# Kernel optimization log

Measured on AMD Instinct MI355X. Metric: run time of the kernel, lower is better.

## Reference

```python
import jax, jax.numpy as jnp
import numpy as np

N_HEADS = 16
HIDDEN = 1024
HEAD_SIZE = HIDDEN // N_HEADS  # 64
BATCH = 2
SEQ_LEN = 2048


def setup_inputs() -> dict:
    key = jax.random.key(0)
    k1, k2, k3 = jax.random.split(key, 3)
    x = jax.random.normal(k1, (BATCH, SEQ_LEN, HIDDEN), dtype=jnp.float32)
    # nn.Linear(hidden, 3*hidden): store weight as [in, out] for x @ W
    W_qkv = jax.random.normal(k2, (HIDDEN, 3 * HIDDEN), dtype=jnp.float32) * (HIDDEN ** -0.5)
    b_qkv = jax.random.normal(k3, (3 * HIDDEN,), dtype=jnp.float32) * 0.02
    return {"x": x, "W_qkv": W_qkv, "b_qkv": b_qkv}


def reference(x, W_qkv, b_qkv):
    B, T, D = x.shape
    nh, hs = N_HEADS, HEAD_SIZE
    scale = hs ** -0.5

    # qkv projection, then the module's exact (unusual) reshape:
    # [B,T,3D] viewed as [3,B,T,hs,nh], permuted to [3,B,nh,T,hs]
    y = x @ W_qkv + b_qkv                      # [B, T, 3D]
    qkv = y.reshape(3, B, T, hs, nh).transpose(0, 1, 4, 2, 3)  # [3,B,nh,T,hs]
    q, k, v = qkv[0], qkv[1], qkv[2]

    # KV-cache scatter with arange index over the full seq is an identity write;
    # cache.transpose(1,2) returns k, v unchanged.

    scores = jnp.einsum('bhtd,bhsd->bhts', q, k) * scale       # [B,nh,T,T]
    causal = jnp.tril(jnp.ones((T, T), dtype=bool))
    scores = jnp.where(causal[None, None], scores, -jnp.inf)
    attn = jax.nn.softmax(scores, axis=-1)
    ctx = jnp.einsum('bhts,bhsd->bhtd', attn, v)               # [B,nh,T,hs]
    # rearrange 'b h t d -> b t (h d)'; note self.o is NOT applied in forward
    return ctx.transpose(0, 2, 1, 3).reshape(B, T, nh * hs)
```

## Files before the change

### kernel.cpp

```cpp
#include <hip/hip_runtime.h>
#include <hip/hip_bf16.h>

typedef __attribute__((ext_vector_type(8))) short s8v;
typedef __attribute__((ext_vector_type(4))) short s4v;
typedef __attribute__((ext_vector_type(4))) float f4v;

__device__ __forceinline__ void g2lds16(const void* g, void* l) {
  __builtin_amdgcn_global_load_lds(
      (__attribute__((address_space(1))) void*)(g),
      (__attribute__((address_space(3))) void*)(l), 16, 0, 0);
}

__device__ __forceinline__ short f2bf(float f) {
  __hip_bfloat16 h = __float2bfloat16(f);
  return *reinterpret_cast<short*>(&h);
}

__global__ void k_prep(const float* __restrict__ x, const float* __restrict__ W,
                       __hip_bfloat16* __restrict__ xb, __hip_bfloat16* __restrict__ Wt) {
  int bx = blockIdx.x;
  if (bx < 4096) {
    int i = (bx * 256 + threadIdx.x) * 4;
    float4 v = *(const float4*)(x + i);
    __hip_bfloat16 o[4] = {__float2bfloat16(v.x), __float2bfloat16(v.y),
                           __float2bfloat16(v.z), __float2bfloat16(v.w)};
    *(uint2*)(xb + i) = *(const uint2*)(o);
  } else {
    __shared__ float tile[32][33];
    int r = bx - 4096;
    int rt = r / 96;
    int ct = r - rt * 96;
    int c0 = ct * 32, r0 = rt * 32;
    int tr = threadIdx.x >> 5, tc = threadIdx.x & 31;
#pragma unroll
    for (int i = 0; i < 32; i += 8)
      tile[tr + i][tc] = W[(size_t)(r0 + tr + i) * 3072 + c0 + tc];
    __syncthreads();
#pragma unroll
    for (int i = 0; i < 32; i += 8)
      Wt[(size_t)(c0 + tr + i) * 1024 + r0 + tc] = __float2bfloat16(tile[tc][tr + i]);
  }
}

__global__ __launch_bounds__(256) void k_gemm(const __hip_bfloat16* __restrict__ A,
                                              const __hip_bfloat16* __restrict__ Bt,
                                              const float* __restrict__ bias,
                                              __hip_bfloat16* __restrict__ Q,
                                              __hip_bfloat16* __restrict__ K,
                                              __hip_bfloat16* __restrict__ Vt) {
  __shared__ __align__(16) __hip_bfloat16 As[2][128 * 32];
  __shared__ __align__(16) __hip_bfloat16 Bs[2][128 * 32];
  const int tid = threadIdx.x;
  const int lane = tid & 63, wave = tid >> 6;
  const int m0 = blockIdx.y * 128, n0 = blockIdx.x * 128;
  const int wm = (wave & 1) * 64, wn = (wave >> 1) * 64;
  const int lrow = lane & 15;
  const int quad = lane >> 4;

  f4v acc[4][4] = {};

  auto stage = [&](int k0, int kb) {
#pragma unroll
    for (int c = 0; c < 2; ++c) {
      int e = c * 2048 + tid * 8;
      int row = e >> 5;
      int slot = (e & 31) >> 3;
      int src = k0 + ((slot ^ ((row >> 1) & 3)) << 3);
      g2lds16(A + (size_t)(m0 + row) * 1024 + src, &As[kb][e]);
      g2lds16(Bt + (size_t)(n0 + row) * 1024 + src, &Bs[kb][e]);
    }
  };

  const int swz = (quad ^ ((lrow >> 1) & 3)) * 8;

  stage(0, 0);
  for (int it = 0; it < 32; ++it) {
    __syncthreads();
    if (it < 31) stage((it + 1) * 32, (it + 1) & 1);
    const __hip_bfloat16* Ab = As[it & 1];
    const __hip_bfloat16* Bb = Bs[it & 1];
    s8v af[4], bfr[4];
#pragma unroll
    for (int mi = 0; mi < 4; ++mi) af[mi] = *(const s8v*)(Ab + (wm + mi * 16 + lrow) * 32 + swz);
#pragma unroll
    for (int ni = 0; ni < 4; ++ni) bfr[ni] = *(const s8v*)(Bb + (wn + ni * 16 + lrow) * 32 + swz);
#pragma unroll
    for (int mi = 0; mi < 4; ++mi)
#pragma unroll
      for (int ni = 0; ni < 4; ++ni)
        acc[mi][ni] = __builtin_amdgcn_mfma_f32_16x16x32_bf16(af[mi], bfr[ni], acc[mi][ni], 0, 0, 0);
  }

  const int cw = n0 + wn;
  const int c10 = cw >> 10;
  const int d0 = (cw & 1023) >> 4;
  const int h = lrow;
  float bv[4];
#pragma unroll
  for (int ni = 0; ni < 4; ++ni) bv[ni] = bias[cw + ni * 16 + lrow];

#pragma unroll
  for (int mi = 0; mi < 4; ++mi) {
    int rbase = m0 + wm + mi * 16 + quad * 4;
#pragma unroll
    for (int reg = 0; reg < 4; ++reg) {
      int rr = rbase + reg;
      int u = 3 * rr + c10;
      int s = u >> 12;
      int b = (u >> 11) & 1;
      int t = u & 2047;
      if (s < 2) {
        __hip_bfloat16* dst = (s == 0) ? Q : K;
        s4v pk;
#pragma unroll
        for (int ni = 0; ni < 4; ++ni) pk[ni] = f2bf(acc[mi][ni][reg] + bv[ni]);
        *(s4v*)(dst + ((size_t)(b * 16 + h) * 2048 + t) * 64 + d0) = pk;
      } else {
#pragma unroll
        for (int ni = 0; ni < 4; ++ni)
          Vt[((size_t)(b * 16 + h) * 64 + d0 + ni) * 2048 + t] =
              __float2bfloat16(acc[mi][ni][reg] + bv[ni]);
      }
    }
  }
}

__global__ __launch_bounds__(256, 3) void k_attn(const __hip_bfloat16* __restrict__ Q,
                                                 const __hip_bfloat16* __restrict__ K,
                                                 const __hip_bfloat16* __restrict__ Vt,
                                                 float* __restrict__ out) {
  __shared__ __align__(16) char lds[2][16384];

  const int tid = threadIdx.x;
  const int lane = tid & 63, w = tid >> 6;
  const int l = lane & 15, q = lane >> 4, lx = l & 7;

  const int bid = blockIdx.x;
  const int xcd = bid & 7;
  const int idx = bid >> 3;
  const int bh = xcd + 8 * (idx & 3);
  const int qb = 31 - (idx >> 2);

  const char* Kb = (const char*)(K + (size_t)bh * 131072);
  const char* Vb = (const char*)(Vt + (size_t)bh * 131072);
  const __hip_bfloat16* Qp = Q + (size_t)bh * 131072 + (size_t)qb * 4096;

  s8v Qf[2];
#pragma unroll
  for (int kh = 0; kh < 2; ++kh)
    Qf[kh] = *(const s8v*)(Qp + (size_t)(w * 16 + l) * 64 + kh * 32 + q * 8);

  f4v O[4] = {};
  float m = -INFINITY, lsum = 0.f;
  const float c1 = 0.125f * 1.44269504088896f;
  const int tg = qb * 64 + w * 16 + l;

  auto stage = [&](int j, char* buf) {
#pragma unroll
    for (int c = 0; c < 4; ++c) {
      int chunk = w * 4 + c;
      int ls = chunk * 64 + lane;
      if (chunk < 8) {
        int row = ls >> 3, kb = ls & 7;
        g2lds16(Kb + (size_t)j * 8192 + row * 128 + ((kb ^ (row & 7)) << 4),
                buf + ls * 16);
      } else {
        int ls2 = ls - 512;
        int d = ls2 >> 3, kb = ls2 & 7;
        g2lds16(Vb + (size_t)d * 4096 + (size_t)j * 128 + ((kb ^ (d & 7)) << 4),
                buf + 8192 + ls2 * 16);
      }
    }
  };

  stage(0, lds[0]);
  __syncthreads();

  for (int j = 0; j <= qb; ++j) {
    const char* Kl = lds[j & 1];
    const char* Vl = Kl + 8192;
    if (j < qb) stage(j + 1, lds[(j + 1) & 1]);

    f4v S[4];
#pragma unroll
    for (int nt = 0; nt < 4; ++nt) {
      const char* rowp = Kl + (nt * 16 + l) * 128;
      s8v k0 = *(const s8v*)(rowp + ((q ^ lx) << 4));
      s8v k1 = *(const s8v*)(rowp + (((4 + q) ^ lx) << 4));
      f4v z = {0.f, 0.f, 0.f, 0.f};
      z = __builtin_amdgcn_mfma_f32_16x16x32_bf16(k0, Qf[0], z, 0, 0, 0);
      z = __builtin_amdgcn_mfma_f32_16x16x32_bf16(k1, Qf[1], z, 0, 0, 0);
      S[nt] = z;
    }

    float p2[4][4];
#pragma unroll
    for (int nt = 0; nt < 4; ++nt)
#pragma unroll
      for (int r = 0; r < 4; ++r) p2[nt][r] = S[nt][r] * c1;
    if (j == qb) {
#pragma unroll
      for (int nt = 0; nt < 4; ++nt)
#pragma unroll
        for (int r = 0; r < 4; ++r)
          if (j * 64 + nt * 16 + q * 4 + r > tg) p2[nt][r] = -1e30f;
    }

    float mx = p2[0][0];
#pragma unroll
    for (int nt = 0; nt < 4; ++nt)
#pragma unroll
      for (int r = 0; r < 4; ++r) mx = fmaxf(mx, p2[nt][r]);
    mx = fmaxf(mx, __shfl_xor(mx, 16));
    mx = fmaxf(mx, __shfl_xor(mx, 32));
    float mn = fmaxf(m, mx);
    float alpha = exp2f(m - mn);
    m = mn;

    float rs = 0.f;
    s4v Pf[4];
#pragma unroll
    for (int nt = 0; nt < 4; ++nt)
#pragma unroll
      for (int r = 0; r < 4; ++r) {
        float e = exp2f(p2[nt][r] - mn);
        rs += e;
        Pf[nt][r] = f2bf(e);
      }
    rs += __shfl_xor(rs, 16);
    rs += __shfl_xor(rs, 32);
    lsum = lsum * alpha + rs;
#pragma unroll
    for (int dt = 0; dt < 4; ++dt) O[dt] *= alpha;

#pragma unroll
    for (int sc = 0; sc < 4; ++sc) {
      int so = ((sc * 2 + (q >> 1)) ^ lx) * 16 + (q & 1) * 8;
#pragma unroll
      for (int dt = 0; dt < 4; ++dt) {
        s4v vv = *(const s4v*)(Vl + (dt * 16 + l) * 128 + so);
        O[dt] = __builtin_amdgcn_mfma_f32_16x16x16bf16_1k(vv, Pf[sc], O[dt], 0, 0, 0);
      }
    }
    __syncthreads();
  }

  float inv = 1.f / lsum;
  int b = bh >> 4, h = bh & 15;
  float* ob = out + ((size_t)b * 2048 + tg) * 1024 + h * 64;
#pragma unroll
  for (int dt = 0; dt < 4; ++dt) {
    f4v val = O[dt] * inv;
    *(f4v*)(ob + dt * 16 + q * 4) = val;
  }
}

extern "C" void kernel_launch(void* const* d_in, const int* in_sizes, int n_in,
                              void* d_out, int out_size, void* d_ws, size_t ws_size,
                              hipStream_t stream) {
  const float* x = (const float*)d_in[0];
  const float* W = (const float*)d_in[1];
  const float* bias = (const float*)d_in[2];
  float* out = (float*)d_out;

  char* ws = (char*)d_ws;
  __hip_bfloat16* xb = (__hip_bfloat16*)ws;
  __hip_bfloat16* Wt = (__hip_bfloat16*)(ws + 8388608);
  __hip_bfloat16* Qg = (__hip_bfloat16*)(ws + 14680064);
  __hip_bfloat16* Kg = (__hip_bfloat16*)(ws + 23068672);
  __hip_bfloat16* Vt = (__hip_bfloat16*)(ws + 31457280);

  k_prep<<<7168, 256, 0, stream>>>(x, W, xb, Wt);
  k_gemm<<<dim3(24, 32), 256, 0, stream>>>(xb, Wt, bias, Qg, Kg, Vt);
  k_attn<<<1024, 256, 0, stream>>>(Qg, Kg, Vt, out);
}
```

Before: 177.1 us.

## Enlarge QKV GEMM tile to 256x256 with 8 waves and interleaved staged pipeline

Result: slower. 188.1 us (+6.2%).

```diff
diff --git a/kernel.cpp b/kernel.cpp
--- a/kernel.cpp
+++ b/kernel.cpp
@@ -15,6 +15,9 @@
   __hip_bfloat16 h = __float2bfloat16(f);
   return *reinterpret_cast<short*>(&h);
 }
+
+#define FENCE asm volatile("" ::: "memory")
+#define BARRIER do { FENCE; __builtin_amdgcn_s_barrier(); FENCE; } while (0)
 
 __global__ void k_prep(const float* __restrict__ x, const float* __restrict__ W,
                        __hip_bfloat16* __restrict__ xb, __hip_bfloat16* __restrict__ Wt) {
@@ -42,53 +45,114 @@
   }
 }
 
-__global__ __launch_bounds__(256) void k_gemm(const __hip_bfloat16* __restrict__ A,
-                                              const __hip_bfloat16* __restrict__ Bt,
-                                              const float* __restrict__ bias,
-                                              __hip_bfloat16* __restrict__ Q,
-                                              __hip_bfloat16* __restrict__ K,
-                                              __hip_bfloat16* __restrict__ Vt) {
-  __shared__ __align__(16) __hip_bfloat16 As[2][128 * 32];
-  __shared__ __align__(16) __hip_bfloat16 Bs[2][128 * 32];
+__global__ __launch_bounds__(512, 2) void k_gemm(const __hip_bfloat16* __restrict__ A,
+                                                 const __hip_bfloat16* __restrict__ Bt,
+                                                 const float* __restrict__ bias,
+                                                 __hip_bfloat16* __restrict__ Q,
+                                                 __hip_bfloat16* __restrict__ K,
+                                                 __hip_bfloat16* __restrict__ Vt) {
+  __shared__ __align__(16) __hip_bfloat16 As[2][256 * 32];
+  __shared__ __align__(16) __hip_bfloat16 Bs[2][256 * 32];
   const int tid = threadIdx.x;
   const int lane = tid & 63, wave = tid >> 6;
-  const int m0 = blockIdx.y * 128, n0 = blockIdx.x * 128;
-  const int wm = (wave & 1) * 64, wn = (wave >> 1) * 64;
-  const int lrow = lane & 15;
-  const int quad = lane >> 4;
-
-  f4v acc[4][4] = {};
-
-  auto stage = [&](int k0, int kb) {
-#pragma unroll
-    for (int c = 0; c < 2; ++c) {
-      int e = c * 2048 + tid * 8;
-      int row = e >> 5;
-      int slot = (e & 31) >> 3;
-      int src = k0 + ((slot ^ ((row >> 1) & 3)) << 3);
-      g2lds16(A + (size_t)(m0 + row) * 1024 + src, &As[kb][e]);
-      g2lds16(Bt + (size_t)(n0 + row) * 1024 + src, &Bs[kb][e]);
-    }
+  const int m0 = blockIdx.y * 256, n0 = blockIdx.x * 256;
+  const int wm = (wave >> 2) * 128;
+  const int wn = (wave & 3) * 64;
+  const int lrow = lane & 15, quad = lane >> 4;
+  const int key = (lrow >> 1) & 3;
+  const int sw8 = (quad ^ key) << 3;
+  const int aPB = (wave >> 2) * 64;
+
+  f4v acc[8][4] = {};
+
+  auto stageA = [&](int kt, int s, int hf) {
+    int e = hf * 4096 + tid * 8;
+    int p = e >> 5;
+    int g = (p & 63) | ((p & 64) << 1) | ((p & 128) >> 1);
+    int oct = (tid & 3) ^ ((p >> 1) & 3);
+    g2lds16(A + (size_t)(m0 + g) * 1024 + kt * 64 + s * 32 + (oct << 3),
+            &As[s][e]);
   };
-
-  const int swz = (quad ^ ((lrow >> 1) & 3)) * 8;
-
-  stage(0, 0);
-  for (int it = 0; it < 32; ++it) {
-    __syncthreads();
-    if (it < 31) stage((it + 1) * 32, (it + 1) & 1);
-    const __hip_bfloat16* Ab = As[it & 1];
-    const __hip_bfloat16* Bb = Bs[it & 1];
+  auto stageB = [&](int kt, int s, int hf) {
+    int e = hf * 4096 + tid * 8;
+    int p = e >> 5;
+    int oct = (tid & 3) ^ ((p >> 1) & 3);
+    g2lds16(Bt + (size_t)(n0 + p) * 1024 + kt * 64 + s * 32 + (oct << 3),
+            &Bs[s][e]);
+  };
+
+  stageA(0, 0, 0); stageA(0, 0, 1); stageB(0, 0, 0); stageB(0, 0, 1);
+  stageA(0, 1, 0); stageA(0, 1, 1); stageB(0, 1, 0); stageB(0, 1, 1);
+  asm volatile("s_waitcnt vmcnt(0)" ::: "memory");
+  BARRIER;
+
+  for (int t = 0; t < 16; ++t) {
+    const int bt = (t < 15) ? t + 1 : 15;
     s8v af[4], bfr[4];
-#pragma unroll
-    for (int mi = 0; mi < 4; ++mi) af[mi] = *(const s8v*)(Ab + (wm + mi * 16 + lrow) * 32 + swz);
-#pragma unroll
-    for (int ni = 0; ni < 4; ++ni) bfr[ni] = *(const s8v*)(Bb + (wn + ni * 16 + lrow) * 32 + swz);
-#pragma unroll
-    for (int mi = 0; mi < 4; ++mi)
-#pragma unroll
-      for (int ni = 0; ni < 4; ++ni)
-        acc[mi][ni] = __builtin_amdgcn_mfma_f32_16x16x32_bf16(af[mi], bfr[ni], acc[mi][ni], 0, 0, 0);
+
+#pragma unroll
+    for (int i = 0; i < 4; ++i)
+      af[i] = *(const s8v*)(&As[0][(aPB + i * 16 + lrow) * 32 + sw8]);
+#pragma unroll
+    for (int i = 0; i < 4; ++i)
+      bfr[i] = *(const s8v*)(&Bs[0][(wn + i * 16 + lrow) * 32 + sw8]);
+    if (t > 0) { stageA(t, 1, 1); stageB(t, 1, 0); stageB(t, 1, 1); }
+    BARRIER;
+    __builtin_amdgcn_s_setprio(1);
+#pragma unroll
+    for (int i = 0; i < 4; ++i)
+#pragma unroll
+      for (int n = 0; n < 4; ++n)
+        acc[i][n] = __builtin_amdgcn_mfma_f32_16x16x32_bf16(af[i], bfr[n], acc[i][n], 0, 0, 0);
+    __builtin_amdgcn_s_setprio(0);
+    BARRIER;
+
+#pragma unroll
+    for (int i = 0; i < 4; ++i)
+      af[i] = *(const s8v*)(&As[0][(aPB + 128 + i * 16 + lrow) * 32 + sw8]);
+    stageA(bt, 0, 0);
+    BARRIER;
+    __builtin_amdgcn_s_setprio(1);
+#pragma unroll
+    for (int i = 0; i < 4; ++i)
+#pragma unroll
+      for (int n = 0; n < 4; ++n)
+        acc[4 + i][n] = __builtin_amdgcn_mfma_f32_16x16x32_bf16(af[i], bfr[n], acc[4 + i][n], 0, 0, 0);
+    __builtin_amdgcn_s_setprio(0);
+    asm volatile("s_waitcnt vmcnt(1)" ::: "memory");
+    BARRIER;
+
+#pragma unroll
+    for (int i = 0; i < 4; ++i)
+      af[i] = *(const s8v*)(&As[1][(aPB + i * 16 + lrow) * 32 + sw8]);
+#pragma unroll
+    for (int i = 0; i < 4; ++i)
+      bfr[i] = *(const s8v*)(&Bs[1][(wn + i * 16 + lrow) * 32 + sw8]);
+    stageA(bt, 0, 1); stageB(bt, 0, 0); stageB(bt, 0, 1);
+    BARRIER;
+    __builtin_amdgcn_s_setprio(1);
+#pragma unroll
+    for (int i = 0; i < 4; ++i)
+#pragma unroll
+      for (int n = 0; n < 4; ++n)
+        acc[i][n] = __builtin_amdgcn_mfma_f32_16x16x32_bf16(af[i], bfr[n], acc[i][n], 0, 0, 0);
+    __builtin_amdgcn_s_setprio(0);
+    BARRIER;
+
+#pragma unroll
+    for (int i = 0; i < 4; ++i)
+      af[i] = *(const s8v*)(&As[1][(aPB + 128 + i * 16 + lrow) * 32 + sw8]);
+    stageA(bt, 1, 0);
+    BARRIER;
+    __builtin_amdgcn_s_setprio(1);
+#pragma unroll
+    for (int i = 0; i < 4; ++i)
+#pragma unroll
+      for (int n = 0; n < 4; ++n)
+        acc[4 + i][n] = __builtin_amdgcn_mfma_f32_16x16x32_bf16(af[i], bfr[n], acc[4 + i][n], 0, 0, 0);
+    __builtin_amdgcn_s_setprio(0);
+    asm volatile("s_waitcnt vmcnt(1)" ::: "memory");
+    BARRIER;
   }
 
   const int cw = n0 + wn;
@@ -100,7 +164,7 @@
   for (int ni = 0; ni < 4; ++ni) bv[ni] = bias[cw + ni * 16 + lrow];
 
 #pragma unroll
-  for (int mi = 0; mi < 4; ++mi) {
+  for (int mi = 0; mi < 8; ++mi) {
     int rbase = m0 + wm + mi * 16 + quad * 4;
 #pragma unroll
     for (int reg = 0; reg < 4; ++reg) {
@@ -108,17 +172,17 @@
       int u = 3 * rr + c10;
       int s = u >> 12;
       int b = (u >> 11) & 1;
-      int t = u & 2047;
+      int tt = u & 2047;
       if (s < 2) {
         __hip_bfloat16* dst = (s == 0) ? Q : K;
         s4v pk;
 #pragma unroll
         for (int ni = 0; ni < 4; ++ni) pk[ni] = f2bf(acc[mi][ni][reg] + bv[ni]);
-        *(s4v*)(dst + ((size_t)(b * 16 + h) * 2048 + t) * 64 + d0) = pk;
+        *(s4v*)(dst + ((size_t)(b * 16 + h) * 2048 + tt) * 64 + d0) = pk;
       } else {
 #pragma unroll
         for (int ni = 0; ni < 4; ++ni)
-          Vt[((size_t)(b * 16 + h) * 64 + d0 + ni) * 2048 + t] =
+          Vt[((size_t)(b * 16 + h) * 64 + d0 + ni) * 2048 + tt] =
               __float2bfloat16(acc[mi][ni][reg] + bv[ni]);
       }
     }
@@ -271,6 +335,6 @@
   __hip_bfloat16* Vt = (__hip_bfloat16*)(ws + 31457280);
 
   k_prep<<<7168, 256, 0, stream>>>(x, W, xb, Wt);
-  k_gemm<<<dim3(24, 32), 256, 0, stream>>>(xb, Wt, bias, Qg, Kg, Vt);
+  k_gemm<<<dim3(12, 16), 512, 0, stream>>>(xb, Wt, bias, Qg, Kg, Vt);
   k_attn<<<1024, 256, 0, stream>>>(Qg, Kg, Vt, out);
 }
```

## Restructure QKV GEMM into 256x256 tiles with phased 8-wave LDS pipeline

Applied to the files above, without the earlier changes.

Measured after the change: 194.1 us. 1.1x slower.

```diff
diff --git a/kernel.cpp b/kernel.cpp
--- a/kernel.cpp
+++ b/kernel.cpp
@@ -15,6 +15,10 @@
   __hip_bfloat16 h = __float2bfloat16(f);
   return *reinterpret_cast<short*>(&h);
 }
+
+#define FENCE asm volatile("" ::: "memory")
+#define BARRIER do { FENCE; __builtin_amdgcn_s_barrier(); FENCE; } while (0)
+#define WAITVM(N) asm volatile("s_waitcnt vmcnt(" #N ")" ::: "memory")
 
 __global__ void k_prep(const float* __restrict__ x, const float* __restrict__ W,
                        __hip_bfloat16* __restrict__ xb, __hip_bfloat16* __restrict__ Wt) {
@@ -42,54 +46,91 @@
   }
 }
 
-__global__ __launch_bounds__(256) void k_gemm(const __hip_bfloat16* __restrict__ A,
-                                              const __hip_bfloat16* __restrict__ Bt,
-                                              const float* __restrict__ bias,
-                                              __hip_bfloat16* __restrict__ Q,
-                                              __hip_bfloat16* __restrict__ K,
-                                              __hip_bfloat16* __restrict__ Vt) {
-  __shared__ __align__(16) __hip_bfloat16 As[2][128 * 32];
-  __shared__ __align__(16) __hip_bfloat16 Bs[2][128 * 32];
+__global__ __launch_bounds__(512, 2) void k_gemm(const __hip_bfloat16* __restrict__ A,
+                                                 const __hip_bfloat16* __restrict__ Bt,
+                                                 const float* __restrict__ bias,
+                                                 __hip_bfloat16* __restrict__ Q,
+                                                 __hip_bfloat16* __restrict__ K,
+                                                 __hip_bfloat16* __restrict__ Vt) {
+  __shared__ __align__(16) __hip_bfloat16 As[2][2][128 * 64];
+  __shared__ __align__(16) __hip_bfloat16 Bs[2][2][128 * 64];
   const int tid = threadIdx.x;
   const int lane = tid & 63, wave = tid >> 6;
-  const int m0 = blockIdx.y * 128, n0 = blockIdx.x * 128;
-  const int wm = (wave & 1) * 64, wn = (wave >> 1) * 64;
-  const int lrow = lane & 15;
-  const int quad = lane >> 4;
-
-  f4v acc[4][4] = {};
-
-  auto stage = [&](int k0, int kb) {
+  const int m0 = blockIdx.y * 256, n0 = blockIdx.x * 256;
+  const int wv2 = wave >> 2;
+  const int wn = (wave & 3) * 64;
+  const int bhi = wn >> 7;
+  const int bRow = wn & 127;
+  const int lrow = lane & 15, quad = lane >> 4;
+  const int lx7 = lrow & 7;
+
+  f4v acc[8][4] = {};
+
+  auto stA = [&](int buf, int h, int kt) {
 #pragma unroll
     for (int c = 0; c < 2; ++c) {
-      int e = c * 2048 + tid * 8;
-      int row = e >> 5;
-      int slot = (e & 31) >> 3;
-      int src = k0 + ((slot ^ ((row >> 1) & 3)) << 3);
-      g2lds16(A + (size_t)(m0 + row) * 1024 + src, &As[kb][e]);
-      g2lds16(Bt + (size_t)(n0 + row) * 1024 + src, &Bs[kb][e]);
+      int e = c * 4096 + tid * 8;
+      int p = e >> 6;
+      int sl = (e >> 3) & 7;
+      g2lds16(A + (size_t)(m0 + h * 128 + p) * 1024 + kt * 64 + ((sl ^ (p & 7)) << 3),
+              &As[buf][h][e]);
     }
   };
-
-  const int swz = (quad ^ ((lrow >> 1) & 3)) * 8;
-
-  stage(0, 0);
-  for (int it = 0; it < 32; ++it) {
-    __syncthreads();
-    if (it < 31) stage((it + 1) * 32, (it + 1) & 1);
-    const __hip_bfloat16* Ab = As[it & 1];
-    const __hip_bfloat16* Bb = Bs[it & 1];
-    s8v af[4], bfr[4];
-#pragma unroll
-    for (int mi = 0; mi < 4; ++mi) af[mi] = *(const s8v*)(Ab + (wm + mi * 16 + lrow) * 32 + swz);
-#pragma unroll
-    for (int ni = 0; ni < 4; ++ni) bfr[ni] = *(const s8v*)(Bb + (wn + ni * 16 + lrow) * 32 + swz);
-#pragma unroll
-    for (int mi = 0; mi < 4; ++mi)
-#pragma unroll
-      for (int ni = 0; ni < 4; ++ni)
-        acc[mi][ni] = __builtin_amdgcn_mfma_f32_16x16x32_bf16(af[mi], bfr[ni], acc[mi][ni], 0, 0, 0);
-  }
+  auto stB = [&](int buf, int h, int kt) {
+#pragma unroll
+    for (int c = 0; c < 2; ++c) {
+      int e = c * 4096 + tid * 8;
+      int p = e >> 6;
+      int sl = (e >> 3) & 7;
+      g2lds16(Bt + (size_t)(n0 + h * 128 + p) * 1024 + kt * 64 + ((sl ^ (p & 7)) << 3),
+              &Bs[buf][h][e]);
+    }
+  };
+
+#define PHASE(BUF, MH, NH, STAGE, GATE) do {                                        \
+    s8v af_[4][2], bf_[2][2];                                                       \
+    _Pragma("unroll") for (int mq = 0; mq < 4; ++mq)                                \
+      _Pragma("unroll") for (int ks = 0; ks < 2; ++ks)                              \
+        af_[mq][ks] = *(const s8v*)(&As[BUF][MH][(wv2 * 64 + mq * 16 + lrow) * 64 + \
+                                                 (((ks * 4 + quad) ^ lx7) << 3)]);  \
+    _Pragma("unroll") for (int nq = 0; nq < 2; ++nq)                                \
+      _Pragma("unroll") for (int ks = 0; ks < 2; ++ks)                              \
+        bf_[nq][ks] = *(const s8v*)(&Bs[BUF][bhi][(bRow + (NH * 2 + nq) * 16 + lrow) * 64 + \
+                                                  (((ks * 4 + quad) ^ lx7) << 3)]); \
+    STAGE                                                                           \
+    BARRIER;                                                                        \
+    asm volatile("s_waitcnt lgkmcnt(0)" ::: "memory");                              \
+    __builtin_amdgcn_sched_barrier(0);                                              \
+    __builtin_amdgcn_s_setprio(1);                                                  \
+    _Pragma("unroll") for (int ks = 0; ks < 2; ++ks)                                \
+      _Pragma("unroll") for (int mq = 0; mq < 4; ++mq)                              \
+        _Pragma("unroll") for (int nq = 0; nq < 2; ++nq)                            \
+          acc[MH * 4 + mq][NH * 2 + nq] = __builtin_amdgcn_mfma_f32_16x16x32_bf16(  \
+              af_[mq][ks], bf_[nq][ks], acc[MH * 4 + mq][NH * 2 + nq], 0, 0, 0);    \
+    __builtin_amdgcn_s_setprio(0);                                                  \
+    GATE                                                                            \
+    BARRIER;                                                                        \
+  } while (0)
+
+  stA(0, 0, 0); stA(0, 1, 0); stB(0, 0, 0); stB(0, 1, 0);
+  stA(1, 0, 1);
+  WAITVM(2);
+  BARRIER;
+
+  for (int i = 0; i < 8; ++i) {
+    const int t1 = 2 * i + 1;
+    const int t2 = (2 * i + 2 < 16) ? 2 * i + 2 : 15;
+    const int t3 = (2 * i + 3 < 16) ? 2 * i + 3 : 15;
+    PHASE(0, 0, 0, { stA(1, 1, t1); stB(1, 0, t1); stB(1, 1, t1); }, );
+    PHASE(0, 0, 1, , );
+    PHASE(0, 1, 0, { stA(0, 0, t2); }, );
+    PHASE(0, 1, 1, , WAITVM(2); );
+    PHASE(1, 0, 0, { stA(0, 1, t2); stB(0, 0, t2); stB(0, 1, t2); }, );
+    PHASE(1, 0, 1, , );
+    PHASE(1, 1, 0, { stA(1, 0, t3); }, );
+    PHASE(1, 1, 1, , WAITVM(2); );
+  }
+#undef PHASE
 
   const int cw = n0 + wn;
   const int c10 = cw >> 10;
@@ -100,25 +141,25 @@
   for (int ni = 0; ni < 4; ++ni) bv[ni] = bias[cw + ni * 16 + lrow];
 
 #pragma unroll
-  for (int mi = 0; mi < 4; ++mi) {
-    int rbase = m0 + wm + mi * 16 + quad * 4;
+  for (int mi = 0; mi < 8; ++mi) {
+    int rbase = m0 + (mi >> 2) * 128 + wv2 * 64 + (mi & 3) * 16 + quad * 4;
 #pragma unroll
     for (int reg = 0; reg < 4; ++reg) {
       int rr = rbase + reg;
       int u = 3 * rr + c10;
       int s = u >> 12;
       int b = (u >> 11) & 1;
-      int t = u & 2047;
+      int tt = u & 2047;
       if (s < 2) {
         __hip_bfloat16* dst = (s == 0) ? Q : K;
         s4v pk;
 #pragma unroll
         for (int ni = 0; ni < 4; ++ni) pk[ni] = f2bf(acc[mi][ni][reg] + bv[ni]);
-        *(s4v*)(dst + ((size_t)(b * 16 + h) * 2048 + t) * 64 + d0) = pk;
+        *(s4v*)(dst + ((size_t)(b * 16 + h) * 2048 + tt) * 64 + d0) = pk;
       } else {
 #pragma unroll
         for (int ni = 0; ni < 4; ++ni)
-          Vt[((size_t)(b * 16 + h) * 64 + d0 + ni) * 2048 + t] =
+          Vt[((size_t)(b * 16 + h) * 64 + d0 + ni) * 2048 + tt] =
               __float2bfloat16(acc[mi][ni][reg] + bv[ni]);
       }
     }
@@ -271,6 +312,6 @@
   __hip_bfloat16* Vt = (__hip_bfloat16*)(ws + 31457280);
 
   k_prep<<<7168, 256, 0, stream>>>(x, W, xb, Wt);
-  k_gemm<<<dim3(24, 32), 256, 0, stream>>>(xb, Wt, bias, Qg, Kg, Vt);
+  k_gemm<<<dim3(12, 16), 512, 0, stream>>>(xb, Wt, bias, Qg, Kg, Vt);
   k_attn<<<1024, 256, 0, stream>>>(Qg, Kg, Vt, out);
 }
```
